# Performance work log

Measured on AMD Instinct MI355X. Metric: run time of the kernel, lower is better.

Reference implementation:

```python
import jax, jax.numpy as jnp
import numpy as np

MODEL_DIM = 1024
NUM_HEADS = 16
DEPTH = MODEL_DIM // NUM_HEADS


def setup_inputs() -> dict:
    key = jax.random.key(0)
    ks = jax.random.split(key, 9)
    B, S, D = 4, 2048, MODEL_DIM
    scale = 1.0 / np.sqrt(D)
    x = jax.random.normal(ks[0], (B, S, D), dtype=jnp.float32)
    wq = jax.random.normal(ks[1], (D, D), dtype=jnp.float32) * scale
    bq = jnp.zeros((D,), dtype=jnp.float32)
    wk = jax.random.normal(ks[2], (D, D), dtype=jnp.float32) * scale
    bk = jnp.zeros((D,), dtype=jnp.float32)
    wv = jax.random.normal(ks[3], (D, D), dtype=jnp.float32) * scale
    bv = jnp.zeros((D,), dtype=jnp.float32)
    wo = jax.random.normal(ks[4], (D, D), dtype=jnp.float32) * scale
    bo = jnp.zeros((D,), dtype=jnp.float32)
    return {"x": x, "wq": wq, "bq": bq, "wk": wk, "bk": bk,
            "wv": wv, "bv": bv, "wo": wo, "bo": bo}


def reference(x, wq, bq, wk, bk, wv, bv, wo, bo):
    B, S, D = x.shape
    H, dh = NUM_HEADS, DEPTH
    # projections
    q = (x @ wq + bq).reshape(B, S, H, dh).transpose(0, 2, 1, 3)  # [B,H,S,dh]
    k = (x @ wk + bk).reshape(B, S, H, dh).transpose(0, 2, 1, 3)
    v = (x @ wv + bv).reshape(B, S, H, dh).transpose(0, 2, 1, 3)
    # scaled dot-product attention (full score matrix, as in source)
    logits = jnp.einsum('bhqd,bhkd->bhqk', q, k) / jnp.sqrt(jnp.float32(dh))
    attn = jax.nn.softmax(logits, axis=-1)
    out = jnp.einsum('bhqk,bhkd->bhqd', attn, v)  # [B,H,S,dh]
    out = out.transpose(0, 2, 1, 3).reshape(B, S, D)
    return out @ wo + bo
```

## Files before the change

kernel.cpp:

```cpp
#include <hip/hip_runtime.h>
#include <hip/hip_bf16.h>


#define S_LEN 2048
#define DMODEL 1024
#define NH 16
#define DH 64
#define BATCH 4
#define MROWS (BATCH * S_LEN)
#define NELEM_X (MROWS * DMODEL)
#define NELEM_W (DMODEL * DMODEL)
#define NELEM_B DMODEL

typedef short short8 __attribute__((ext_vector_type(8)));
typedef float floatx4 __attribute__((ext_vector_type(4)));

__device__ __forceinline__ float bf2f(unsigned short u) {
    union { unsigned int i; float f; } c; c.i = ((unsigned int)u) << 16; return c.f;
}
__device__ __forceinline__ unsigned int f2bf_pk(float lo, float hi) {
    unsigned int r;
    asm("v_cvt_pk_bf16_f32 %0, %1, %2" : "=v"(r) : "v"(lo), "v"(hi));
    return r;
}
__device__ __forceinline__ void async_copy16(const void* g, void* l) {
    __builtin_amdgcn_global_load_lds(
        (const __attribute__((address_space(1))) unsigned int*)g,
        (__attribute__((address_space(3))) unsigned int*)l, 16, 0, 0);
}

__global__ void sniff_kernel(const unsigned short* __restrict__ x, int* flag) {
    __shared__ int cnt;
    if (threadIdx.x == 0) cnt = 0;
    __syncthreads();
    int c = 0;
    for (int i = threadIdx.x; i < 65536; i += 256) {
        unsigned int e = (x[i] >> 7) & 0xFFu;
        if (e >= 0xC0u) c++;
    }
    atomicAdd(&cnt, c);
    __syncthreads();
    if (threadIdx.x == 0) *flag = (cnt > 64) ? 1 : 0;
}

struct ConvArgs { const void* s[5]; unsigned short* d[5]; int n8[5]; };
__global__ void convert_all(ConvArgs a, const int* __restrict__ flag) {
    const int seg = blockIdx.y;
    const int f = *flag;
    const int n8 = a.n8[seg];
    unsigned short* dst = a.d[seg];
    int i = blockIdx.x * blockDim.x + threadIdx.x;
    const int stride = gridDim.x * blockDim.x;
    if (f) {
        const float4* s4 = (const float4*)a.s[seg];
        for (; i < n8; i += stride) {
            float4 x0 = s4[2 * i], x1 = s4[2 * i + 1];
            uint4 o;
            o.x = f2bf_pk(x0.x, x0.y); o.y = f2bf_pk(x0.z, x0.w);
            o.z = f2bf_pk(x1.x, x1.y); o.w = f2bf_pk(x1.z, x1.w);
            *(uint4*)(dst + (size_t)i * 8) = o;
        }
    } else {
        const uint4* s4 = (const uint4*)a.s[seg];
        for (; i < n8; i += stride) *(uint4*)(dst + (size_t)i * 8) = s4[i];
    }
}

struct TWArgs { const void* s[4]; unsigned short* d[4]; };
__global__ void transpose_w(TWArgs a, const int* __restrict__ flag) {
    __shared__ unsigned int Lt[64 * 33];
    const int z = blockIdx.z;
    const int f = *flag;
    const int k0 = blockIdx.x * 64, n0 = blockIdx.y * 64;
    const int t = threadIdx.x;
    const int c = t & 63, rgrp = t >> 6;

    if (f) {
        const float* W = (const float*)a.s[z];
        #pragma unroll
        for (int s = 0; s < 8; s++) {
            int r0 = rgrp * 16 + 2 * s;
            float v0 = W[(size_t)(k0 + r0) * DMODEL + n0 + c];
            float v1 = W[(size_t)(k0 + r0 + 1) * DMODEL + n0 + c];
            Lt[c * 33 + rgrp * 8 + s] = f2bf_pk(v0, v1);
        }
    } else {
        const unsigned short* W = (const unsigned short*)a.s[z];
        #pragma unroll
        for (int s = 0; s < 8; s++) {
            int r0 = rgrp * 16 + 2 * s;
            unsigned int lo = W[(size_t)(k0 + r0) * DMODEL + n0 + c];
            unsigned int hi = W[(size_t)(k0 + r0 + 1) * DMODEL + n0 + c];
            Lt[c * 33 + rgrp * 8 + s] = lo | (hi << 16);
        }
    }
    __syncthreads();
    const int row = t >> 2, j = t & 3;
    unsigned int* outp = (unsigned int*)(a.d[z] + (size_t)(n0 + row) * DMODEL + k0);
    #pragma unroll
    for (int i = 0; i < 8; i++) outp[j * 8 + i] = Lt[row * 33 + j * 8 + i];
}

__global__ void transpose_v(const unsigned short* __restrict__ vws,
                            unsigned short* __restrict__ vt) {
    __shared__ unsigned int Lt[64 * 33];
    const int tok0 = blockIdx.x * 64;
    const int bh   = blockIdx.y;
    const int b    = bh >> 4;
    const int h    = bh & 15;
    const int t = threadIdx.x;
    const int c = t & 63, rgrp = t >> 6;

    const unsigned short* src = vws + (size_t)b * S_LEN * DMODEL + h * DH;
    #pragma unroll
    for (int s = 0; s < 8; s++) {
        int r0 = rgrp * 16 + 2 * s;
        unsigned int lo = src[(size_t)(tok0 + r0) * DMODEL + c];
        unsigned int hi = src[(size_t)(tok0 + r0 + 1) * DMODEL + c];
        Lt[c * 33 + rgrp * 8 + s] = lo | (hi << 16);
    }
    __syncthreads();
    const int row = t >> 2, j = t & 3;
    unsigned int* outp = (unsigned int*)(vt + (size_t)bh * DH * S_LEN
                                            + (size_t)row * S_LEN + tok0);
    #pragma unroll
    for (int i = 0; i < 8; i++) outp[j * 8 + i] = Lt[row * 33 + j * 8 + i];
}

__global__ __launch_bounds__(256, 2)
void gemm_bias_kernel(const unsigned short* __restrict__ X,
                      const unsigned short* __restrict__ T0, const unsigned short* __restrict__ B0, void* __restrict__ Y0,
                      const unsigned short* __restrict__ T1, const unsigned short* __restrict__ B1, void* __restrict__ Y1,
                      const unsigned short* __restrict__ T2, const unsigned short* __restrict__ B2, void* __restrict__ Y2,
                      float os0, float os1, float os2,
                      const int* __restrict__ flag, int fp32_out)
{
    const unsigned short* Wt = T0; const unsigned short* Bi = B0; void* Y = Y0;
    float os = os0;
    if (blockIdx.z == 1) { Wt = T1; Bi = B1; Y = Y1; os = os1; }
    else if (blockIdx.z == 2) { Wt = T2; Bi = B2; Y = Y2; os = os2; }
    const int f32o = fp32_out ? (*flag) : 0;

    __shared__ __align__(16) unsigned short As[128 * 32];
    __shared__ __align__(16) unsigned short Bs[128 * 32];

    const int t    = threadIdx.x;
    const int lane = t & 63;
    const int wid  = t >> 6;
    const int quad = lane >> 4;
    const int n16  = lane & 15;
    const int wm   = wid >> 1, wn = wid & 1;

    const int m0 = blockIdx.x * 128;
    const int n0 = blockIdx.y * 128;

    floatx4 acc[4][4];
    #pragma unroll
    for (int i = 0; i < 4; i++)
        #pragma unroll
        for (int j = 0; j < 4; j++) acc[i][j] = (floatx4){0.f, 0.f, 0.f, 0.f};

    const int r = t >> 2, c8 = (t & 3) * 8;

    for (int kb = 0; kb < DMODEL; kb += 32) {
        __syncthreads();
        async_copy16(X  + (size_t)(m0 + r)      * DMODEL + kb + c8, As + r * 32 + c8);
        async_copy16(X  + (size_t)(m0 + 64 + r) * DMODEL + kb + c8, As + (64 + r) * 32 + c8);
        async_copy16(Wt + (size_t)(n0 + r)      * DMODEL + kb + c8, Bs + r * 32 + c8);
        async_copy16(Wt + (size_t)(n0 + 64 + r) * DMODEL + kb + c8, Bs + (64 + r) * 32 + c8);
        __syncthreads();

        short8 af[4], bfr[4];
        #pragma unroll
        for (int mt = 0; mt < 4; mt++)
            af[mt] = *(const short8*)(As + (wm * 64 + mt * 16 + n16) * 32 + quad * 8);
        #pragma unroll
        for (int nt = 0; nt < 4; nt++)
            bfr[nt] = *(const short8*)(Bs + (wn * 64 + nt * 16 + n16) * 32 + quad * 8);
        #pragma unroll
        for (int mt = 0; mt < 4; mt++)
            #pragma unroll
            for (int nt = 0; nt < 4; nt++)
                acc[mt][nt] = __builtin_amdgcn_mfma_f32_16x16x32_bf16(af[mt], bfr[nt], acc[mt][nt], 0, 0, 0);
    }

    float bv4[4];
    #pragma unroll
    for (int nt = 0; nt < 4; nt++) bv4[nt] = bf2f(Bi[n0 + wn * 64 + nt * 16 + n16]) * os;
    #pragma unroll
    for (int mt = 0; mt < 4; mt++)
        #pragma unroll
        for (int rr = 0; rr < 4; rr++) {
            size_t row = (size_t)(m0 + wm * 64 + mt * 16 + quad * 4 + rr);
            if (f32o) {
                #pragma unroll
                for (int nt = 0; nt < 4; nt++) {
                    int col = n0 + wn * 64 + nt * 16 + n16;
                    ((float*)Y)[row * DMODEL + col] = fmaf(acc[mt][nt][rr], os, bv4[nt]);
                }
            } else {
                #pragma unroll
                for (int np = 0; np < 2; np++) {
                    float v0 = fmaf(acc[mt][2 * np    ][rr], os, bv4[2 * np]);
                    float v1 = fmaf(acc[mt][2 * np + 1][rr], os, bv4[2 * np + 1]);
                    unsigned int pk = f2bf_pk(v0, v1);
                    int col = n0 + wn * 64 + (2 * np) * 16 + n16;
                    ((unsigned short*)Y)[row * DMODEL + col]      = (unsigned short)pk;
                    ((unsigned short*)Y)[row * DMODEL + col + 16] = (unsigned short)(pk >> 16);
                }
            }
        }
}

__global__ __launch_bounds__(256, 2)
void attn_kernel(const unsigned short* Qw,
                 const unsigned short* __restrict__ Kw,
                 const unsigned short* __restrict__ VT,
                 unsigned short* Ow)
{
    __shared__ __align__(16) unsigned short Ks[64 * 72];
    __shared__ __align__(16) unsigned short Vts[64 * 72];
    __shared__ __align__(16) unsigned short Ps[4 * 16 * 72];

    const int t    = threadIdx.x;
    const int lane = t & 63;
    const int w    = t >> 6;
    const int quad = lane >> 4;
    const int n16  = lane & 15;

    const int bid  = blockIdx.x;
    const int bh   = bid & 63;
    const int qblk = bid >> 6;
    const int b    = bh >> 4;
    const int h    = bh & 15;

    const size_t baseRow = (size_t)b * S_LEN;
    const int hoff = h * DH;
    const unsigned short* VTb = VT + (size_t)bh * DH * S_LEN;

    int qrow[4];
    short8 qf[4][2];
    #pragma unroll
    for (int g = 0; g < 4; g++) {
        qrow[g] = qblk * 256 + w * 64 + g * 16 + n16;
        qf[g][0] = *(const short8*)(Qw + (baseRow + qrow[g]) * DMODEL + hoff + quad * 8);
        qf[g][1] = *(const short8*)(Qw + (baseRow + qrow[g]) * DMODEL + hoff + 32 + quad * 8);
    }

    floatx4 acco[4][4];
    #pragma unroll
    for (int g = 0; g < 4; g++)
        #pragma unroll
        for (int i = 0; i < 4; i++) acco[g][i] = (floatx4){0.f, 0.f, 0.f, 0.f};
    float ls[4] = {0.f, 0.f, 0.f, 0.f};

    const int krow = t >> 3, kchk = (t & 7) * 8;
    const int vrow = t >> 2, vchk = (t & 3) * 16;

    for (int kb = 0; kb < S_LEN; kb += 64) {
        __syncthreads();
        *(float4*)(Ks + krow * 72 + kchk) =
            *(const float4*)(Kw + (baseRow + kb + krow) * DMODEL + hoff + kchk);
        *(float4*)(Ks + (krow + 32) * 72 + kchk) =
            *(const float4*)(Kw + (baseRow + kb + krow + 32) * DMODEL + hoff + kchk);
        *(float4*)(Vts + vrow * 72 + vchk) =
            *(const float4*)(VTb + (size_t)vrow * S_LEN + kb + vchk);
        *(float4*)(Vts + vrow * 72 + vchk + 8) =
            *(const float4*)(VTb + (size_t)vrow * S_LEN + kb + vchk + 8);
        __syncthreads();

        floatx4 sf[4][4];
        #pragma unroll
        for (int g = 0; g < 4; g++)
            #pragma unroll
            for (int kt = 0; kt < 4; kt++) sf[g][kt] = (floatx4){0.f, 0.f, 0.f, 0.f};
        #pragma unroll
        for (int kt = 0; kt < 4; kt++)
            #pragma unroll
            for (int ks = 0; ks < 2; ks++) {
                short8 kf = *(const short8*)(Ks + (kt * 16 + n16) * 72 + ks * 32 + quad * 8);
                #pragma unroll
                for (int g = 0; g < 4; g++)
                    sf[g][kt] = __builtin_amdgcn_mfma_f32_16x16x32_bf16(kf, qf[g][ks], sf[g][kt], 0, 0, 0);
            }

        unsigned short* Pw = Ps + w * 16 * 72;
        unsigned int*   Pu = (unsigned int*)Pw;
        short8 pf[4][2];
        #pragma unroll
        for (int g = 0; g < 4; g++) {
            float lsum = 0.f;
            #pragma unroll
            for (int kt = 0; kt < 4; kt++)
                #pragma unroll
                for (int rr = 0; rr < 4; rr++) {
                    float p = __builtin_exp2f(sf[g][kt][rr]);
                    sf[g][kt][rr] = p;
                    lsum += p;
                }
            ls[g] += lsum;
            #pragma unroll
            for (int kt = 0; kt < 4; kt++) {
                uint2 pk2 = make_uint2(f2bf_pk(sf[g][kt][0], sf[g][kt][1]),
                                       f2bf_pk(sf[g][kt][2], sf[g][kt][3]));
                *(uint2*)(Pu + n16 * 36 + kt * 8 + quad * 2) = pk2;
            }
            __asm__ volatile("" ::: "memory");
            pf[g][0] = *(const short8*)(Pw + n16 * 72 + quad * 8);
            pf[g][1] = *(const short8*)(Pw + n16 * 72 + 32 + quad * 8);
            __asm__ volatile("" ::: "memory");
        }

        #pragma unroll
        for (int ks = 0; ks < 2; ks++)
            #pragma unroll
            for (int dt = 0; dt < 4; dt++) {
                short8 vf = *(const short8*)(Vts + (dt * 16 + n16) * 72 + ks * 32 + quad * 8);
                #pragma unroll
                for (int g = 0; g < 4; g++)
                    acco[g][dt] = __builtin_amdgcn_mfma_f32_16x16x32_bf16(vf, pf[g][ks], acco[g][dt], 0, 0, 0);
            }
    }

    #pragma unroll
    for (int g = 0; g < 4; g++) {
        float l = ls[g];
        l += __shfl_xor(l, 16);
        l += __shfl_xor(l, 32);
        const float rinv = 1.f / l;
        #pragma unroll
        for (int dt = 0; dt < 4; dt++) {
            uint2 o;
            o.x = f2bf_pk(acco[g][dt][0] * rinv, acco[g][dt][1] * rinv);
            o.y = f2bf_pk(acco[g][dt][2] * rinv, acco[g][dt][3] * rinv);
            *(uint2*)(Ow + (baseRow + qrow[g]) * DMODEL + hoff + dt * 16 + quad * 4) = o;
        }
    }
}

extern "C" void kernel_launch(void* const* d_in, const int* in_sizes, int n_in,
                              void* d_out, int out_size, void* d_ws, size_t ws_size,
                              hipStream_t stream)
{
    unsigned short* base = (unsigned short*)d_ws;
    int* flag = (int*)d_ws;
    unsigned short* xc  = base + 8;
    unsigned short* wqt = xc  + NELEM_X;
    unsigned short* wkt = wqt + NELEM_W;
    unsigned short* wvt = wkt + NELEM_W;
    unsigned short* wot = wvt + NELEM_W;
    unsigned short* bqc = wot + NELEM_W;
    unsigned short* bkc = bqc + NELEM_B;
    unsigned short* bvc = bkc + NELEM_B;
    unsigned short* boc = bvc + NELEM_B;
    unsigned short* qws = boc + NELEM_B;
    unsigned short* kws = qws + NELEM_X;
    unsigned short* vws = kws + NELEM_X;
    unsigned short* aws = qws;
    unsigned short* vtw = xc;

    sniff_kernel<<<1, 256, 0, stream>>>((const unsigned short*)d_in[0], flag);

    ConvArgs ca;
    const void* csrc[5] = {d_in[0], d_in[2], d_in[4], d_in[6], d_in[8]};
    unsigned short* cdst[5] = {xc, bqc, bkc, bvc, boc};
    int cn8[5] = {NELEM_X / 8, NELEM_B / 8, NELEM_B / 8, NELEM_B / 8, NELEM_B / 8};
    for (int i = 0; i < 5; i++) { ca.s[i] = csrc[i]; ca.d[i] = cdst[i]; ca.n8[i] = cn8[i]; }
    convert_all<<<dim3(256, 5), 256, 0, stream>>>(ca, flag);

    TWArgs tw;
    const void* tsrc[4] = {d_in[1], d_in[3], d_in[5], d_in[7]};
    unsigned short* tdst[4] = {wqt, wkt, wvt, wot};
    for (int i = 0; i < 4; i++) { tw.s[i] = tsrc[i]; tw.d[i] = tdst[i]; }
    transpose_w<<<dim3(16, 16, 4), 256, 0, stream>>>(tw, flag);

    const float qscale = 0.125f * 1.44269504088896340736f;
    gemm_bias_kernel<<<dim3(64, 8, 3), 256, 0, stream>>>(
        xc, wqt, bqc, qws, wkt, bkc, kws, wvt, bvc, vws,
        qscale, 1.f, 1.f, flag, 0);

    transpose_v<<<dim3(32, 64), 256, 0, stream>>>(vws, vtw);

    attn_kernel<<<dim3(512), 256, 0, stream>>>(qws, kws, vtw, aws);

    gemm_bias_kernel<<<dim3(64, 8, 1), 256, 0, stream>>>(
        aws, wot, boc, d_out, wot, boc, d_out, wot, boc, d_out,
        1.f, 1.f, 1.f, flag, 1);
}
```

Before: 406.3 us.

## Prefetch next K/V tile into registers and batch P staging in attention

The attention loop now loads the next K and V tiles from global memory into registers while the current tile is being computed, so global latency overlaps with MFMA work. The P staging buffer grows to hold all four row groups per wave, which allows all bf16 stores and then all reloads to be batched instead of interleaved. s_setprio is raised around the MFMA sections to favour matrix issue. This costs more LDS per block (about 55KB total) and more registers, which may reduce occupancy below the two blocks per CU requested by launch bounds.

```diff
diff --git a/kernel.cpp b/kernel.cpp
--- a/kernel.cpp
+++ b/kernel.cpp
@@ -220,7 +220,7 @@
 {
     __shared__ __align__(16) unsigned short Ks[64 * 72];
     __shared__ __align__(16) unsigned short Vts[64 * 72];
-    __shared__ __align__(16) unsigned short Ps[4 * 16 * 72];
+    __shared__ __align__(16) unsigned short Ps[4 * 64 * 72];
 
     const int t    = threadIdx.x;
     const int lane = t & 63;
@@ -257,16 +257,27 @@
     const int krow = t >> 3, kchk = (t & 7) * 8;
     const int vrow = t >> 2, vchk = (t & 3) * 16;
 
+    const unsigned short* Kp0 = Kw + (baseRow + krow)      * DMODEL + hoff + kchk;
+    const unsigned short* Kp1 = Kw + (baseRow + krow + 32) * DMODEL + hoff + kchk;
+    const unsigned short* Vp  = VTb + (size_t)vrow * S_LEN + vchk;
+
+    float4 kr0 = *(const float4*)(Kp0);
+    float4 kr1 = *(const float4*)(Kp1);
+    float4 vr0 = *(const float4*)(Vp);
+    float4 vr1 = *(const float4*)(Vp + 8);
+
     for (int kb = 0; kb < S_LEN; kb += 64) {
         __syncthreads();
-        *(float4*)(Ks + krow * 72 + kchk) =
-            *(const float4*)(Kw + (baseRow + kb + krow) * DMODEL + hoff + kchk);
-        *(float4*)(Ks + (krow + 32) * 72 + kchk) =
-            *(const float4*)(Kw + (baseRow + kb + krow + 32) * DMODEL + hoff + kchk);
-        *(float4*)(Vts + vrow * 72 + vchk) =
-            *(const float4*)(VTb + (size_t)vrow * S_LEN + kb + vchk);
-        *(float4*)(Vts + vrow * 72 + vchk + 8) =
-            *(const float4*)(VTb + (size_t)vrow * S_LEN + kb + vchk + 8);
+        *(float4*)(Ks + krow * 72 + kchk)        = kr0;
+        *(float4*)(Ks + (krow + 32) * 72 + kchk) = kr1;
+        *(float4*)(Vts + vrow * 72 + vchk)       = vr0;
+        *(float4*)(Vts + vrow * 72 + vchk + 8)   = vr1;
+        if (kb + 64 < S_LEN) {
+            kr0 = *(const float4*)(Kp0 + (size_t)(kb + 64) * DMODEL);
+            kr1 = *(const float4*)(Kp1 + (size_t)(kb + 64) * DMODEL);
+            vr0 = *(const float4*)(Vp + kb + 64);
+            vr1 = *(const float4*)(Vp + kb + 72);
+        }
         __syncthreads();
 
         floatx4 sf[4][4];
@@ -274,6 +285,7 @@
         for (int g = 0; g < 4; g++)
             #pragma unroll
             for (int kt = 0; kt < 4; kt++) sf[g][kt] = (floatx4){0.f, 0.f, 0.f, 0.f};
+        __builtin_amdgcn_s_setprio(1);
         #pragma unroll
         for (int kt = 0; kt < 4; kt++)
             #pragma unroll
@@ -283,10 +295,8 @@
                 for (int g = 0; g < 4; g++)
                     sf[g][kt] = __builtin_amdgcn_mfma_f32_16x16x32_bf16(kf, qf[g][ks], sf[g][kt], 0, 0, 0);
             }
-
-        unsigned short* Pw = Ps + w * 16 * 72;
-        unsigned int*   Pu = (unsigned int*)Pw;
-        short8 pf[4][2];
+        __builtin_amdgcn_s_setprio(0);
+
         #pragma unroll
         for (int g = 0; g < 4; g++) {
             float lsum = 0.f;
@@ -299,18 +309,28 @@
                     lsum += p;
                 }
             ls[g] += lsum;
+        }
+
+        unsigned short* Pw = Ps + w * 64 * 72;
+        unsigned int*   Pu = (unsigned int*)Pw;
+        #pragma unroll
+        for (int g = 0; g < 4; g++)
             #pragma unroll
             for (int kt = 0; kt < 4; kt++) {
                 uint2 pk2 = make_uint2(f2bf_pk(sf[g][kt][0], sf[g][kt][1]),
                                        f2bf_pk(sf[g][kt][2], sf[g][kt][3]));
-                *(uint2*)(Pu + n16 * 36 + kt * 8 + quad * 2) = pk2;
+                *(uint2*)(Pu + (g * 16 + n16) * 36 + kt * 8 + quad * 2) = pk2;
             }
-            __asm__ volatile("" ::: "memory");
-            pf[g][0] = *(const short8*)(Pw + n16 * 72 + quad * 8);
-            pf[g][1] = *(const short8*)(Pw + n16 * 72 + 32 + quad * 8);
-            __asm__ volatile("" ::: "memory");
-        }
-
+        __asm__ volatile("" ::: "memory");
+        short8 pf[4][2];
+        #pragma unroll
+        for (int g = 0; g < 4; g++) {
+            pf[g][0] = *(const short8*)(Pw + (g * 16 + n16) * 72 + quad * 8);
+            pf[g][1] = *(const short8*)(Pw + (g * 16 + n16) * 72 + 32 + quad * 8);
+        }
+        __asm__ volatile("" ::: "memory");
+
+        __builtin_amdgcn_s_setprio(1);
         #pragma unroll
         for (int ks = 0; ks < 2; ks++)
             #pragma unroll
@@ -320,6 +340,7 @@
                 for (int g = 0; g < 4; g++)
                     acco[g][dt] = __builtin_amdgcn_mfma_f32_16x16x32_bf16(vf, pf[g][ks], acco[g][dt], 0, 0, 0);
             }
+        __builtin_amdgcn_s_setprio(0);
     }
 
     #pragma unroll
```

Result: faster. 394.5 us (-2.9%).
